# Kernel tuning notes

Measured on AMD Instinct MI355X. Metric: run time of the kernel, lower is better.

Reference implementation:

```python
import jax, jax.numpy as jnp
import numpy as np

SIZE = (128, 128, 128)  # volume dims (X, Y, Z)
B, N, C = 2, 2097152, 1


def setup_inputs() -> dict:
    key = jax.random.key(0)
    k1, k2 = jax.random.split(key)
    image = jax.random.normal(k1, (B, SIZE[0], SIZE[1], SIZE[2], C), dtype=jnp.float32)
    grid = jax.random.uniform(k2, (B, N, 3), dtype=jnp.float32)  # normalized coords in [0,1]
    return {"image": image, "grid": grid}


def reference(image, grid):
    # image: [B, X, Y, Z, C]; grid: [B, N, 3] normalized -> trilinear sample -> [B, N, C]
    factor = jnp.array(SIZE, dtype=jnp.float32)
    idx = jnp.clip(grid * factor, 0.001, float(min(SIZE)) - 1.001)  # [B, N, 3]
    x, y, z = idx[..., 0], idx[..., 1], idx[..., 2]
    x1, x2 = jnp.floor(x), jnp.ceil(x)
    y1, y2 = jnp.floor(y), jnp.ceil(y)
    z1, z2 = jnp.floor(z), jnp.ceil(z)

    b = jnp.arange(image.shape[0])[:, None]  # [B, 1] batch index for gathers

    def g(xi, yi, zi):  # corner gather -> [B, N, C]
        return image[b, xi.astype(jnp.int32), yi.astype(jnp.int32), zi.astype(jnp.int32)]

    wx, wx2 = (x - x1)[..., None], (x2 - x)[..., None]
    wy, wy2 = (y - y1)[..., None], (y2 - y)[..., None]
    wz, wz2 = (z - z1)[..., None], (z2 - z)[..., None]

    lerp_y1 = (g(x2, y1, z1) * wx + g(x1, y1, z1) * wx2) * wy2 \
            + (g(x2, y2, z1) * wx + g(x1, y2, z1) * wx2) * wy
    lerp_y2 = (g(x2, y1, z2) * wx + g(x1, y1, z2) * wx2) * wy2 \
            + (g(x2, y2, z2) * wx + g(x1, y2, z2) * wx2) * wy
    return lerp_y2 * wz + lerp_y1 * wz2
```

## Files before the change

kernel.cpp:

```cpp
#include <hip/hip_runtime.h>
#include <hip/hip_fp16.h>


#define TOTAL   (2 * 2097152)
#define LOG2N   21
#define VOL     (128 * 128 * 128)
#define NVOX    (2 * VOL)
#define SPB     4

__global__ __launch_bounds__(256)
void ImageWarped_cvt_fp16_kernel(const float* __restrict__ in,
                                 __half* __restrict__ out)
{
    const int i = blockIdx.x * 256 + threadIdx.x;
    const float4 v = ((const float4*)in)[i];
    union { __half2 h2[2]; uint2 u; } p;
    p.h2[0] = __floats2half2_rn(v.x, v.y);
    p.h2[1] = __floats2half2_rn(v.z, v.w);
    ((uint2*)out)[i] = p.u;
}

__global__ __launch_bounds__(256)
void ImageWarped_trilinear_h4_kernel(const __half* __restrict__ image,
                                     const float* __restrict__ grid,
                                     float* __restrict__ out)
{
    const int batch = blockIdx.x & 1;
    const int t     = (blockIdx.x >> 1) * 256 + threadIdx.x;
    const int i0    = (batch << LOG2N) | (t << 2);

    const float4* __restrict__ G4 = (const float4*)grid;
    const int fb = (3 * i0) >> 2;
    const float4 ga = G4[fb + 0];
    const float4 gb = G4[fb + 1];
    const float4 gc = G4[fb + 2];

    const float cx[SPB] = { ga.x, ga.w, gb.z, gc.y };
    const float cy[SPB] = { ga.y, gb.x, gb.w, gc.z };
    const float cz[SPB] = { ga.z, gb.y, gc.x, gc.w };

    const __half* __restrict__ img = image + ((size_t)batch << LOG2N);

    float wxa[SPB], wx2a[SPB], wya[SPB], wy2a[SPB], wza[SPB], wz2a[SPB];
    int   sha[SPB];
    uint2 w11[SPB], w21[SPB], w12[SPB], w22[SPB];

    #pragma unroll
    for (int k = 0; k < SPB; ++k) {
        const float xf = fminf(fmaxf(cx[k] * 128.0f, 0.001f), 126.999f);
        const float yf = fminf(fmaxf(cy[k] * 128.0f, 0.001f), 126.999f);
        const float zf = fminf(fmaxf(cz[k] * 128.0f, 0.001f), 126.999f);

        const float x1f = floorf(xf), x2f = ceilf(xf);
        const float y1f = floorf(yf), y2f = ceilf(yf);
        const float z1f = floorf(zf), z2f = ceilf(zf);

        wxa[k] = xf - x1f;  wx2a[k] = x2f - xf;
        wya[k] = yf - y1f;  wy2a[k] = y2f - yf;
        wza[k] = zf - z1f;  wz2a[k] = z2f - zf;

        const int bx1 = ((int)x1f) << 14, bx2 = ((int)x2f) << 14;
        const int by1 = ((int)y1f) << 7,  by2 = ((int)y2f) << 7;
        const int iz1 = (int)z1f;

        const int ze = min(iz1 & ~1, 124);
        sha[k] = (iz1 - ze) << 4;

        const __half* p = img + ze;
        w11[k] = *(const uint2*)(p + bx1 + by1);
        w21[k] = *(const uint2*)(p + bx2 + by1);
        w12[k] = *(const uint2*)(p + bx1 + by2);
        w22[k] = *(const uint2*)(p + bx2 + by2);
    }

    float res[SPB];
    #pragma unroll
    for (int k = 0; k < SPB; ++k) {
        auto zl = [&](uint2 u) -> float {
            unsigned long long w = ((unsigned long long)u.y << 32) | u.x;
            w >>= sha[k];
            union { unsigned int u32; __half2 h; } c;
            c.u32 = (unsigned int)w;
            const float2 f = __half22float2(c.h);
            return f.x * wz2a[k] + f.y * wza[k];
        };
        const float q11 = zl(w11[k]);
        const float q21 = zl(w21[k]);
        const float q12 = zl(w12[k]);
        const float q22 = zl(w22[k]);
        res[k] = (q21 * wxa[k] + q11 * wx2a[k]) * wy2a[k]
               + (q22 * wxa[k] + q12 * wx2a[k]) * wya[k];
    }

    float4 o; o.x = res[0]; o.y = res[1]; o.z = res[2]; o.w = res[3];
    ((float4*)out)[i0 >> 2] = o;
}

__global__ __launch_bounds__(256)
void ImageWarped_trilinear_f_kernel(const float* __restrict__ image,
                                    const float* __restrict__ grid,
                                    float* __restrict__ out)
{
    const int i = blockIdx.x * 256 + threadIdx.x;
    if (i >= TOTAL) return;
    const float gx = grid[3 * i + 0];
    const float gy = grid[3 * i + 1];
    const float gz = grid[3 * i + 2];
    const float* __restrict__ img = image + ((size_t)(i >> LOG2N) << LOG2N);

    const float xf = fminf(fmaxf(gx * 128.0f, 0.001f), 126.999f);
    const float yf = fminf(fmaxf(gy * 128.0f, 0.001f), 126.999f);
    const float zf = fminf(fmaxf(gz * 128.0f, 0.001f), 126.999f);

    const float x1f = floorf(xf), x2f = ceilf(xf);
    const float y1f = floorf(yf), y2f = ceilf(yf);
    const float z1f = floorf(zf), z2f = ceilf(zf);
    const float wx = xf - x1f, wx2 = x2f - xf;
    const float wy = yf - y1f, wy2 = y2f - yf;
    const float wz = zf - z1f, wz2 = z2f - zf;

    const int bx1 = ((int)x1f) << 14, bx2 = ((int)x2f) << 14;
    const int by1 = ((int)y1f) << 7,  by2 = ((int)y2f) << 7;
    const int iz1 = (int)z1f,         iz2 = (int)z2f;

    const float c111 = img[bx1 + by1 + iz1], c211 = img[bx2 + by1 + iz1];
    const float c121 = img[bx1 + by2 + iz1], c221 = img[bx2 + by2 + iz1];
    const float c112 = img[bx1 + by1 + iz2], c212 = img[bx2 + by1 + iz2];
    const float c122 = img[bx1 + by2 + iz2], c222 = img[bx2 + by2 + iz2];

    const float l1 = (c211 * wx + c111 * wx2) * wy2 + (c221 * wx + c121 * wx2) * wy;
    const float l2 = (c212 * wx + c112 * wx2) * wy2 + (c222 * wx + c122 * wx2) * wy;
    out[i] = l2 * wz + l1 * wz2;
}

extern "C" void kernel_launch(void* const* d_in, const int* in_sizes, int n_in,
                              void* d_out, int out_size, void* d_ws, size_t ws_size,
                              hipStream_t stream)
{
    const float* image = (const float*)d_in[0];
    const float* grid  = (const float*)d_in[1];
    float* out = (float*)d_out;

    if (ws_size >= (size_t)NVOX * sizeof(__half)) {
        __half* img16 = (__half*)d_ws;
        ImageWarped_cvt_fp16_kernel<<<NVOX / 4 / 256, 256, 0, stream>>>(image, img16);
        ImageWarped_trilinear_h4_kernel<<<TOTAL / (256 * SPB), 256, 0, stream>>>(
            img16, grid, out);
    } else {
        ImageWarped_trilinear_f_kernel<<<TOTAL / 256, 256, 0, stream>>>(image, grid, out);
    }
}
```

Baseline: 174.7 us.

## Repack volume into y4×z8 fp16 bricks to cut gather count per sample

Replaces the flat fp16 conversion with a repack kernel that stores the volume as bricks of 4 y by 8 z halves, with y innermost per z slot. The sampler loads one 16-byte vector per x plane when y and z neighbors fall in the same brick, falling back to extra 8-byte loads across brick boundaries. This aims to reduce the number of scattered memory transactions per trilinear sample, at the cost of data-dependent branching and a more complex repack pass.

Result: slower. 179.7 us (+2.8%).

```diff
diff --git a/kernel.cpp b/kernel.cpp
--- a/kernel.cpp
+++ b/kernel.cpp
@@ -8,22 +8,98 @@
 #define NVOX    (2 * VOL)
 #define SPB     4
 
+typedef unsigned long long u64;
+typedef unsigned int       u32;
+
 __global__ __launch_bounds__(256)
-void ImageWarped_cvt_fp16_kernel(const float* __restrict__ in,
-                                 __half* __restrict__ out)
-{
-    const int i = blockIdx.x * 256 + threadIdx.x;
-    const float4 v = ((const float4*)in)[i];
-    union { __half2 h2[2]; uint2 u; } p;
-    p.h2[0] = __floats2half2_rn(v.x, v.y);
-    p.h2[1] = __floats2half2_rn(v.z, v.w);
-    ((uint2*)out)[i] = p.u;
+void ImageWarped_repack_kernel(const float* __restrict__ in,
+                               __half* __restrict__ out)
+{
+    const int t  = blockIdx.x * 256 + threadIdx.x;
+    const int zb = t & 15;
+    const int yb = (t >> 4) & 31;
+    const int x  = (t >> 9) & 127;
+    const int b  = t >> 16;
+
+    const float* src = in + ((size_t)b << 21) + (x << 14)
+                          + ((yb << 2) << 7) + (zb << 3);
+
+    unsigned short h[32];
+    #pragma unroll
+    for (int yi = 0; yi < 4; ++yi) {
+        const float4 lo = *(const float4*)(src + (yi << 7));
+        const float4 hi = *(const float4*)(src + (yi << 7) + 4);
+        h[ 0 + yi] = __half_as_ushort(__float2half_rn(lo.x));
+        h[ 4 + yi] = __half_as_ushort(__float2half_rn(lo.y));
+        h[ 8 + yi] = __half_as_ushort(__float2half_rn(lo.z));
+        h[12 + yi] = __half_as_ushort(__float2half_rn(lo.w));
+        h[16 + yi] = __half_as_ushort(__float2half_rn(hi.x));
+        h[20 + yi] = __half_as_ushort(__float2half_rn(hi.y));
+        h[24 + yi] = __half_as_ushort(__float2half_rn(hi.z));
+        h[28 + yi] = __half_as_ushort(__float2half_rn(hi.w));
+    }
+
+    u32 w[16];
+    #pragma unroll
+    for (int j = 0; j < 16; ++j)
+        w[j] = (u32)h[2 * j] | ((u32)h[2 * j + 1] << 16);
+
+    uint4* dst = (uint4*)(out + (size_t)t * 32);
+    dst[0] = make_uint4(w[0],  w[1],  w[2],  w[3]);
+    dst[1] = make_uint4(w[4],  w[5],  w[6],  w[7]);
+    dst[2] = make_uint4(w[8],  w[9],  w[10], w[11]);
+    dst[3] = make_uint4(w[12], w[13], w[14], w[15]);
+}
+
+__device__ __forceinline__ float col_get(u64 c, int yi)
+{
+    return __half2float(__ushort_as_half((unsigned short)(c >> (yi << 4))));
+}
+
+__device__ __forceinline__ float plane_sample(const __half* __restrict__ imgt,
+                                              int x,
+                                              int yb1, int yi1, int yb2, int yi2,
+                                              int zb1, int zi1, int zb2, int zi2,
+                                              float wz, float wz2,
+                                              float wy, float wy2)
+{
+    const int tb = (x << 5) | yb1;
+    const __half* p1 = imgt + (size_t)(((tb << 4) | zb1) << 5);
+
+    u64 colz1, colz2;
+    if (zb1 == zb2) {
+        const uint4 q = *(const uint4*)(p1 + (zi1 << 2));
+        colz1 = ((u64)q.y << 32) | q.x;
+        colz2 = (zi2 == zi1) ? colz1 : (((u64)q.w << 32) | q.z);
+    } else {
+        colz1 = *(const u64*)(p1 + (zi1 << 2));
+        const __half* p2 = imgt + (size_t)(((tb << 4) | zb2) << 5);
+        colz2 = *(const u64*)(p2 + (zi2 << 2));
+    }
+
+    const float vy1z1 = col_get(colz1, yi1);
+    const float vy1z2 = col_get(colz2, yi1);
+
+    float vy2z1, vy2z2;
+    if (yb2 == yb1) {
+        vy2z1 = col_get(colz1, yi2);
+        vy2z2 = col_get(colz2, yi2);
+    } else {
+        const int tc = (x << 5) | yb2;
+        const u64 b1 = *(const u64*)(imgt + (size_t)(((tc << 4) | zb1) << 5) + (zi1 << 2));
+        const u64 b2 = *(const u64*)(imgt + (size_t)(((tc << 4) | zb2) << 5) + (zi2 << 2));
+        vy2z1 = col_get(b1, yi2);
+        vy2z2 = col_get(b2, yi2);
+    }
+
+    return (vy1z1 * wz2 + vy1z2 * wz) * wy2
+         + (vy2z1 * wz2 + vy2z2 * wz) * wy;
 }
 
 __global__ __launch_bounds__(256)
-void ImageWarped_trilinear_h4_kernel(const __half* __restrict__ image,
-                                     const float* __restrict__ grid,
-                                     float* __restrict__ out)
+void ImageWarped_trilinear_t_kernel(const __half* __restrict__ imgt,
+                                    const float* __restrict__ grid,
+                                    float* __restrict__ out)
 {
     const int batch = blockIdx.x & 1;
     const int t     = (blockIdx.x >> 1) * 256 + threadIdx.x;
@@ -35,61 +111,42 @@
     const float4 gb = G4[fb + 1];
     const float4 gc = G4[fb + 2];
 
-    const float cx[SPB] = { ga.x, ga.w, gb.z, gc.y };
-    const float cy[SPB] = { ga.y, gb.x, gb.w, gc.z };
-    const float cz[SPB] = { ga.z, gb.y, gc.x, gc.w };
-
-    const __half* __restrict__ img = image + ((size_t)batch << LOG2N);
-
-    float wxa[SPB], wx2a[SPB], wya[SPB], wy2a[SPB], wza[SPB], wz2a[SPB];
-    int   sha[SPB];
-    uint2 w11[SPB], w21[SPB], w12[SPB], w22[SPB];
-
+    const float cxs[SPB] = { ga.x, ga.w, gb.z, gc.y };
+    const float cys[SPB] = { ga.y, gb.x, gb.w, gc.z };
+    const float czs[SPB] = { ga.z, gb.y, gc.x, gc.w };
+
+    const __half* __restrict__ img = imgt + ((size_t)batch << LOG2N);
+
+    float res[SPB];
     #pragma unroll
     for (int k = 0; k < SPB; ++k) {
-        const float xf = fminf(fmaxf(cx[k] * 128.0f, 0.001f), 126.999f);
-        const float yf = fminf(fmaxf(cy[k] * 128.0f, 0.001f), 126.999f);
-        const float zf = fminf(fmaxf(cz[k] * 128.0f, 0.001f), 126.999f);
+        const float xf = fminf(fmaxf(cxs[k] * 128.0f, 0.001f), 126.999f);
+        const float yf = fminf(fmaxf(cys[k] * 128.0f, 0.001f), 126.999f);
+        const float zf = fminf(fmaxf(czs[k] * 128.0f, 0.001f), 126.999f);
 
         const float x1f = floorf(xf), x2f = ceilf(xf);
         const float y1f = floorf(yf), y2f = ceilf(yf);
         const float z1f = floorf(zf), z2f = ceilf(zf);
 
-        wxa[k] = xf - x1f;  wx2a[k] = x2f - xf;
-        wya[k] = yf - y1f;  wy2a[k] = y2f - yf;
-        wza[k] = zf - z1f;  wz2a[k] = z2f - zf;
-
-        const int bx1 = ((int)x1f) << 14, bx2 = ((int)x2f) << 14;
-        const int by1 = ((int)y1f) << 7,  by2 = ((int)y2f) << 7;
-        const int iz1 = (int)z1f;
-
-        const int ze = min(iz1 & ~1, 124);
-        sha[k] = (iz1 - ze) << 4;
-
-        const __half* p = img + ze;
-        w11[k] = *(const uint2*)(p + bx1 + by1);
-        w21[k] = *(const uint2*)(p + bx2 + by1);
-        w12[k] = *(const uint2*)(p + bx1 + by2);
-        w22[k] = *(const uint2*)(p + bx2 + by2);
-    }
-
-    float res[SPB];
-    #pragma unroll
-    for (int k = 0; k < SPB; ++k) {
-        auto zl = [&](uint2 u) -> float {
-            unsigned long long w = ((unsigned long long)u.y << 32) | u.x;
-            w >>= sha[k];
-            union { unsigned int u32; __half2 h; } c;
-            c.u32 = (unsigned int)w;
-            const float2 f = __half22float2(c.h);
-            return f.x * wz2a[k] + f.y * wza[k];
-        };
-        const float q11 = zl(w11[k]);
-        const float q21 = zl(w21[k]);
-        const float q12 = zl(w12[k]);
-        const float q22 = zl(w22[k]);
-        res[k] = (q21 * wxa[k] + q11 * wx2a[k]) * wy2a[k]
-               + (q22 * wxa[k] + q12 * wx2a[k]) * wya[k];
+        const float wx = xf - x1f, wx2 = x2f - xf;
+        const float wy = yf - y1f, wy2 = y2f - yf;
+        const float wz = zf - z1f, wz2 = z2f - zf;
+
+        const int ix1 = (int)x1f, ix2 = (int)x2f;
+        const int iy1 = (int)y1f, iy2 = (int)y2f;
+        const int iz1 = (int)z1f, iz2 = (int)z2f;
+
+        const int yb1 = iy1 >> 2, yi1 = iy1 & 3;
+        const int yb2 = iy2 >> 2, yi2 = iy2 & 3;
+        const int zb1 = iz1 >> 3, zi1 = iz1 & 7;
+        const int zb2 = iz2 >> 3, zi2 = iz2 & 7;
+
+        const float r1 = plane_sample(img, ix1, yb1, yi1, yb2, yi2,
+                                      zb1, zi1, zb2, zi2, wz, wz2, wy, wy2);
+        const float r2 = plane_sample(img, ix2, yb1, yi1, yb2, yi2,
+                                      zb1, zi1, zb2, zi2, wz, wz2, wy, wy2);
+
+        res[k] = r2 * wx + r1 * wx2;
     }
 
     float4 o; o.x = res[0]; o.y = res[1]; o.z = res[2]; o.w = res[3];
@@ -141,11 +198,11 @@
     const float* grid  = (const float*)d_in[1];
     float* out = (float*)d_out;
 
-    if (ws_size >= (size_t)NVOX * sizeof(__half)) {
-        __half* img16 = (__half*)d_ws;
-        ImageWarped_cvt_fp16_kernel<<<NVOX / 4 / 256, 256, 0, stream>>>(image, img16);
-        ImageWarped_trilinear_h4_kernel<<<TOTAL / (256 * SPB), 256, 0, stream>>>(
-            img16, grid, out);
+    if (ws_size >= (size_t)NVOX * sizeof(__half) + 64) {
+        __half* imgt = (__half*)d_ws;
+        ImageWarped_repack_kernel<<<512, 256, 0, stream>>>(image, imgt);
+        ImageWarped_trilinear_t_kernel<<<TOTAL / (256 * SPB), 256, 0, stream>>>(
+            imgt, grid, out);
     } else {
         ImageWarped_trilinear_f_kernel<<<TOTAL / 256, 256, 0, stream>>>(image, grid, out);
     }
```
